# Kernel tuning notes

Hardware: AMD Instinct MI355X
Metric: run time of the kernel (lower is better)

Reference implementation:

```python
import jax, jax.numpy as jnp
from jax import lax
import numpy as np

COST_CLASS, COST_BOX, COST_GIOU = 1.0, 5.0, 2.0
B, Q, C, T = 16, 900, 92, 100
INF = jnp.float32(1e18)


def setup_inputs() -> dict:
    key = jax.random.key(0)
    k1, k2, k3, k4 = jax.random.split(key, 4)
    pred_logits = jax.random.normal(k1, (B, Q, C), jnp.float32)

    def mk_boxes(k, n):
        kc, ks = jax.random.split(k)
        cxcy = jax.random.uniform(kc, (B, n, 2), jnp.float32) * 0.8 + 0.1
        wh = jax.random.uniform(ks, (B, n, 2), jnp.float32) * 0.2 + 0.05
        return jnp.concatenate([cxcy, wh], axis=-1)  # valid cxcywh in (0,1)

    pred_boxes = mk_boxes(k2, Q)
    tgt_boxes = mk_boxes(k3, T)
    tgt_labels = jax.random.randint(k4, (B, T), 0, C)
    return {"pred_logits": pred_logits, "pred_boxes": pred_boxes,
            "tgt_labels": tgt_labels, "tgt_boxes": tgt_boxes}


def box_cxcywh_to_xyxy(b):
    cx, cy, w, h = b[..., 0], b[..., 1], b[..., 2], b[..., 3]
    return jnp.stack([cx - 0.5 * w, cy - 0.5 * h, cx + 0.5 * w, cy + 0.5 * h], axis=-1)


def generalized_box_iou(a, b):
    # a: [B,Q,4] xyxy, b: [B,T,4] xyxy -> [B,Q,T]
    area_a = (a[..., 2] - a[..., 0]) * (a[..., 3] - a[..., 1])  # [B,Q]
    area_b = (b[..., 2] - b[..., 0]) * (b[..., 3] - b[..., 1])  # [B,T]
    a_ = a[:, :, None, :]
    b_ = b[:, None, :, :]
    lt = jnp.maximum(a_[..., :2], b_[..., :2])
    rb = jnp.minimum(a_[..., 2:], b_[..., 2:])
    wh = jnp.clip(rb - lt, 0.0)
    inter = wh[..., 0] * wh[..., 1]
    union = area_a[:, :, None] + area_b[:, None, :] - inter
    iou = inter / union
    lt_c = jnp.minimum(a_[..., :2], b_[..., :2])
    rb_c = jnp.maximum(a_[..., 2:], b_[..., 2:])
    wh_c = jnp.clip(rb_c - lt_c, 0.0)
    area_c = wh_c[..., 0] * wh_c[..., 1]
    return iou - (area_c - union) / area_c


def cost_matrix(pred_logits, pred_boxes, tgt_labels, tgt_boxes):
    probs = jax.nn.softmax(pred_logits, axis=-1)                         # [B,Q,C]
    cost_class = -jnp.take_along_axis(probs, tgt_labels[:, None, :], 2)  # [B,Q,T]
    cost_box = jnp.abs(pred_boxes[:, :, None, :] - tgt_boxes[:, None, :, :]).sum(-1)
    cost_giou = -generalized_box_iou(box_cxcywh_to_xyxy(pred_boxes),
                                     box_cxcywh_to_xyxy(tgt_boxes))
    return COST_BOX * cost_box + COST_CLASS * cost_class + COST_GIOU * cost_giou


def hungarian(cost):
    # Jonker-Volgenant shortest augmenting path. cost: [n, m], n <= m, minimize.
    # Returns col_for_row [n]: column assigned to each row.
    n, m = cost.shape

    def solve_row(i, uvp):
        u, v, p = uvp  # u:[n+1] row potentials, v:[m+1] col potentials, p:[m+1] col->row (n = free)
        p = p.at[m].set(i)  # virtual start column holds current row
        minv = jnp.full((m,), INF, jnp.float32)
        way = jnp.zeros((m,), jnp.int32)
        used = jnp.zeros((m + 1,), bool)
        j0 = jnp.int32(m)

        def cond(s):
            _, _, _, _, _, j0 = s
            return p[j0] != n  # stop when a free column is reached

        def body(s):
            u, v, minv, way, used, j0 = s
            used = used.at[j0].set(True)
            i0 = p[j0]
            cur = cost[i0] - u[i0] - v[:m]           # reduced costs of row i0
            mask = (~used[:m]) & (cur < minv)
            minv = jnp.where(mask, cur, minv)
            way = jnp.where(mask, j0, way)
            mvals = jnp.where(used[:m], INF, minv)
            j1 = jnp.argmin(mvals).astype(jnp.int32)
            delta = mvals[j1]
            u = u.at[p].add(jnp.where(used, delta, 0.0))
            v = v - jnp.where(used, delta, 0.0)
            minv = jnp.where(used[:m], minv, minv - delta)
            return (u, v, minv, way, used, j1)

        u, v, minv, way, used, j0 = lax.while_loop(cond, body, (u, v, minv, way, used, j0))

        def acond(s):
            _, j0 = s
            return j0 != m

        def abody(s):
            p, j0 = s
            j1 = way[j0]
            p = p.at[j0].set(p[j1])
            return (p, j1)

        p, _ = lax.while_loop(acond, abody, (p, j0))
        return (u, v, p)

    u0 = jnp.zeros((n + 1,), jnp.float32)
    v0 = jnp.zeros((m + 1,), jnp.float32)
    p0 = jnp.full((m + 1,), n, jnp.int32)
    _, _, p = lax.fori_loop(0, n, solve_row, (u0, v0, p0))
    col_for_row = jnp.zeros((n + 1,), jnp.int32).at[p[:m]].set(
        jnp.arange(m, dtype=jnp.int32))[:n]
    return col_for_row


def reference(pred_logits, pred_boxes, tgt_labels, tgt_boxes):
    cost = cost_matrix(pred_logits, pred_boxes, tgt_labels, tgt_boxes)  # [B,Q,T]
    # assign each target (row) to a distinct query (col); vmap over batch
    q_per_t = jax.vmap(hungarian)(jnp.swapaxes(cost, 1, 2))  # [B,T]
    order = jnp.argsort(q_per_t, axis=-1)                    # sort by query idx (scipy convention)
    q_idx = jnp.take_along_axis(q_per_t, order, axis=-1)     # query indices  [B,T]
    t_idx = order.astype(jnp.int32)                          # target indices [B,T]
    return cost, q_idx, t_idx
```

## Files before the change

kernel.cpp:

```cpp
#include <hip/hip_runtime.h>

#define BB 16
#define QQ 900
#define QP 960
#define VIRT QP
#define CC 92
#define TT 100
#define INFF 1e18f
#define NK 15

#define DPP_STEP_F(x, ctrl, OP)                                             \
  do {                                                                      \
    float _o = __int_as_float(__builtin_amdgcn_update_dpp(                  \
        __float_as_int(x), __float_as_int(x), (ctrl), 0xF, 0xF, false));    \
    (x) = OP((x), _o);                                                      \
  } while (0)

#define DPP_STEP_I(x, ctrl)                                                 \
  do {                                                                      \
    int _o = __builtin_amdgcn_update_dpp((x), (x), (ctrl), 0xF, 0xF, false);\
    (x) = ((_o) < (x)) ? (_o) : (x);                                        \
  } while (0)

__device__ __forceinline__ float wave_fmin63(float x) {
  DPP_STEP_F(x, 0xB1, fminf);
  DPP_STEP_F(x, 0x4E, fminf);
  DPP_STEP_F(x, 0x141, fminf);
  DPP_STEP_F(x, 0x140, fminf);
  DPP_STEP_F(x, 0x142, fminf);
  DPP_STEP_F(x, 0x143, fminf);
  return x;
}
__device__ __forceinline__ float wave_fmax63(float x) {
  DPP_STEP_F(x, 0xB1, fmaxf);
  DPP_STEP_F(x, 0x4E, fmaxf);
  DPP_STEP_F(x, 0x141, fmaxf);
  DPP_STEP_F(x, 0x140, fmaxf);
  DPP_STEP_F(x, 0x142, fmaxf);
  DPP_STEP_F(x, 0x143, fmaxf);
  return x;
}
__device__ __forceinline__ float wave_fadd63(float x) {
#define ADDF(a, b) ((a) + (b))
  DPP_STEP_F(x, 0xB1, ADDF);
  DPP_STEP_F(x, 0x4E, ADDF);
  DPP_STEP_F(x, 0x141, ADDF);
  DPP_STEP_F(x, 0x140, ADDF);
  DPP_STEP_F(x, 0x142, ADDF);
  DPP_STEP_F(x, 0x143, ADDF);
#undef ADDF
  return x;
}
__device__ __forceinline__ int wave_imin63(int x) {
  DPP_STEP_I(x, 0xB1);
  DPP_STEP_I(x, 0x4E);
  DPP_STEP_I(x, 0x141);
  DPP_STEP_I(x, 0x140);
  DPP_STEP_I(x, 0x142);
  DPP_STEP_I(x, 0x143);
  return x;
}

__global__ __launch_bounds__(64) void cost_kernel(
    const float* __restrict__ logits,
    const float* __restrict__ pboxes,
    const int*   __restrict__ tlabels,
    const float* __restrict__ tboxes,
    float* __restrict__ cost,
    float* __restrict__ costT,
    int ctp)
{
  const int bq   = blockIdx.x;
  const int b    = bq / QQ;
  const int q    = bq - b * QQ;
  const int lane = threadIdx.x;

  __shared__ float sl[CC];

  const float a = logits[(size_t)bq * CC + lane];
  const float bb2 = (lane < CC - 64)
                        ? logits[(size_t)bq * CC + 64 + lane]
                        : -3.402823466e38f;

  float mx = fmaxf(a, bb2);
  mx = wave_fmax63(mx);
  const float m = __int_as_float(
      __builtin_amdgcn_readlane(__float_as_int(mx), 63));

  const float e0 = expf(a - m);
  const float e1 = (lane < CC - 64) ? expf(bb2 - m) : 0.0f;
  sl[lane] = e0;
  if (lane < CC - 64) sl[64 + lane] = e1;

  float sm = e0 + e1;
  sm = wave_fadd63(sm);
  const float ssum = __int_as_float(
      __builtin_amdgcn_readlane(__float_as_int(sm), 63));

  const float4 pbv = ((const float4*)pboxes)[bq];
  const float pax1 = pbv.x - 0.5f * pbv.z, pay1 = pbv.y - 0.5f * pbv.w;
  const float pax2 = pbv.x + 0.5f * pbv.z, pay2 = pbv.y + 0.5f * pbv.w;
  const float area_a = (pax2 - pax1) * (pay2 - pay1);

  for (int t = lane; t < TT; t += 64) {
    const int lab = tlabels[b * TT + t];
    const float cc = -(sl[lab] / ssum);

    const float4 tb = ((const float4*)tboxes)[b * TT + t];
    const float cbox = fabsf(pbv.x - tb.x) + fabsf(pbv.y - tb.y) +
                       fabsf(pbv.z - tb.z) + fabsf(pbv.w - tb.w);

    const float bx1 = tb.x - 0.5f * tb.z, by1 = tb.y - 0.5f * tb.w;
    const float bx2 = tb.x + 0.5f * tb.z, by2 = tb.y + 0.5f * tb.w;
    const float area_b = (bx2 - bx1) * (by2 - by1);

    const float ltx = fmaxf(pax1, bx1), lty = fmaxf(pay1, by1);
    const float rbx = fminf(pax2, bx2), rby = fminf(pay2, by2);
    const float iw = fmaxf(rbx - ltx, 0.0f), ih = fmaxf(rby - lty, 0.0f);
    const float inter = iw * ih;
    const float uni = area_a + area_b - inter;
    const float iou = inter / uni;

    const float cx1 = fminf(pax1, bx1), cy1 = fminf(pay1, by1);
    const float cx2 = fmaxf(pax2, bx2), cy2 = fmaxf(pay2, by2);
    const float cw = fmaxf(cx2 - cx1, 0.0f), ch = fmaxf(cy2 - cy1, 0.0f);
    const float ac = cw * ch;
    const float giou = iou - (ac - uni) / ac;

    const float cval = 5.0f * cbox + cc - 2.0f * giou;
    cost[(size_t)bq * TT + t] = cval;
    if (ctp) costT[((size_t)b * TT + t) * ctp + q] = cval;
  }
  if (ctp == QP && q < QP - QQ) {
    for (int t = lane; t < TT; t += 64)
      costT[((size_t)b * TT + t) * QP + QQ + q] = INFF;
  }
}

__global__ void __launch_bounds__(64, 1)
__attribute__((amdgpu_waves_per_eu(1)))
hungarianT_kernel(
    const float* __restrict__ ct,
    float* __restrict__ out_q,
    float* __restrict__ out_t)
{
  const int b    = blockIdx.x;
  const int lane = threadIdx.x;

  __shared__ int p_lds[QP + 1];
  __shared__ int way_lds[QP];
  __shared__ int qpt[TT];

  const float* __restrict__ base = ct + (size_t)b * TT * QP;

  for (int j = lane; j <= QP; j += 64) p_lds[j] = TT;

  float u0 = 0.0f, u1 = 0.0f;
  float v[NK];
#pragma unroll
  for (int k = 0; k < NK; ++k) v[k] = 0.0f;

  float c[NK];
#pragma unroll
  for (int k = 0; k < NK; ++k) c[k] = base[k * 64 + lane];

  for (int i = 0; i < TT; ++i) {
    p_lds[VIRT] = i;

    float minv[NK];
#pragma unroll
    for (int k = 0; k < NK; ++k) minv[k] = INFF;
    unsigned umask = 0;
    bool t0 = false, t1 = false;

    int i0 = i;
    int j0 = VIRT;
    int jfin;

    float us = (i0 < 64) ? u0 : u1;
    float ui0 = __int_as_float(
        __builtin_amdgcn_readlane(__float_as_int(us), i0 & 63));

    while (true) {
      t0 = t0 || (i0 == lane);
      t1 = t1 || (i0 == 64 + lane);
      if (j0 != VIRT && (j0 & 63) == lane) umask |= (1u << (j0 >> 6));

      float lmin  = INFF;
      int   kbest = 0;
#pragma unroll
      for (int k = 0; k < NK; ++k) {
        const bool  uk  = (umask >> k) & 1u;
        const float cur = c[k] - ui0 - v[k];
        const bool  imp = !uk && (cur < minv[k]);
        if (imp) { minv[k] = cur; way_lds[k * 64 + lane] = j0; }
        const float eff = uk ? INFF : minv[k];
        if (eff < lmin) { lmin = eff; kbest = k; }
      }
      const int lidx = kbest * 64 + lane;

      float red = wave_fmin63(lmin);
      const float delta = __int_as_float(
          __builtin_amdgcn_readlane(__float_as_int(red), 63));
      int cand = (lmin == delta) ? lidx : 0x7FFFFFFF;
      int redi = wave_imin63(cand);
      const int j1 = __builtin_amdgcn_readlane(redi, 63);

      int i0n = p_lds[j1];
      i0n = __builtin_amdgcn_readfirstlane(i0n);
      const bool fin = (i0n == TT);

      if (!fin) {
        const float* __restrict__ row = base + (size_t)i0n * QP;
#pragma unroll
        for (int k = 0; k < NK; ++k) c[k] = row[k * 64 + lane];
      }

      u0 += t0 ? delta : 0.0f;
      u1 += t1 ? delta : 0.0f;
#pragma unroll
      for (int k = 0; k < NK; ++k) {
        const bool uk = (umask >> k) & 1u;
        v[k]    -= uk ? delta : 0.0f;
        minv[k] -= uk ? 0.0f  : delta;
      }

      if (fin) { jfin = j1; break; }
      float us2 = (i0n < 64) ? u0 : u1;
      ui0 = __int_as_float(
          __builtin_amdgcn_readlane(__float_as_int(us2), i0n & 63));
      j0 = j1;
      i0 = i0n;
    }

    if (i + 1 < TT) {
      const float* __restrict__ row = base + (size_t)(i + 1) * QP;
#pragma unroll
      for (int k = 0; k < NK; ++k) c[k] = row[k * 64 + lane];
    }

    int j = jfin;
    while (j != VIRT) {
      const int jn = way_lds[j];
      const int pj = p_lds[jn];
      p_lds[j] = pj;
      j = jn;
    }
    asm volatile("" ::: "memory");
  }

#pragma unroll
  for (int k = 0; k < NK; ++k) {
    const int j = k * 64 + lane;
    const int r = p_lds[j];
    if (r < TT) qpt[r] = j;
  }
  __syncthreads();

  for (int t = lane; t < TT; t += 64) {
    const int myq = qpt[t];
    int rank = 0;
    for (int t2 = 0; t2 < TT; ++t2) rank += (qpt[t2] < myq) ? 1 : 0;
    out_q[b * TT + rank] = (float)myq;
    out_t[b * TT + rank] = (float)t;
  }
}

__global__ void __launch_bounds__(64)
hungarian_kernel(
    const float* __restrict__ cost,
    const float* __restrict__ costT,
    float* __restrict__ out_q,
    float* __restrict__ out_t)
{
  const int b    = blockIdx.x;
  const int lane = threadIdx.x;

  __shared__ int p_lds[QQ + 1];
  __shared__ int way_lds[QQ];
  __shared__ int qpt[TT];

  const float* base;
  size_t rs, cs;
  if (costT) { base = costT + (size_t)b * TT * QQ; rs = QQ; cs = 1; }
  else       { base = cost  + (size_t)b * QQ * TT; rs = 1;  cs = TT; }

  for (int j = lane; j <= QQ; j += 64) p_lds[j] = TT;

  float u0 = 0.0f, u1 = 0.0f;
  float v[NK];
#pragma unroll
  for (int k = 0; k < NK; ++k) v[k] = 0.0f;

  float c[NK];
#pragma unroll
  for (int k = 0; k < NK; ++k) {
    const int j = k * 64 + lane;
    c[k] = (j < QQ) ? base[(size_t)j * cs] : 0.0f;
  }

  for (int i = 0; i < TT; ++i) {
    p_lds[QQ] = i;

    float minv[NK];
#pragma unroll
    for (int k = 0; k < NK; ++k) minv[k] = INFF;
    unsigned umask = 0;
    bool t0 = false, t1 = false;

    int i0 = i;
    int j0 = QQ;
    int jfin;

    float us = (i0 < 64) ? u0 : u1;
    float ui0 = __int_as_float(
        __builtin_amdgcn_readlane(__float_as_int(us), i0 & 63));

    while (true) {
      t0 = t0 || (i0 == lane);
      t1 = t1 || (i0 == 64 + lane);
      if (j0 != QQ) {
        if ((j0 & 63) == lane) umask |= (1u << (j0 >> 6));
      }

      float lmin = INFF;
      int   lidx = QQ;
#pragma unroll
      for (int k = 0; k < NK; ++k) {
        const int j = k * 64 + lane;
        if (j < QQ && !((umask >> k) & 1u)) {
          const float cur = c[k] - ui0 - v[k];
          if (cur < minv[k]) { minv[k] = cur; way_lds[j] = j0; }
          if (minv[k] < lmin) { lmin = minv[k]; lidx = j; }
        }
      }

      float red = wave_fmin63(lmin);
      const float delta = __int_as_float(
          __builtin_amdgcn_readlane(__float_as_int(red), 63));
      int cand = (lmin == delta) ? lidx : 0x7FFFFFFF;
      int redi = wave_imin63(cand);
      const int j1 = __builtin_amdgcn_readlane(redi, 63);

      int i0n = p_lds[j1];
      i0n = __builtin_amdgcn_readfirstlane(i0n);
      const bool fin = (i0n == TT);

      u0 += t0 ? delta : 0.0f;
      u1 += t1 ? delta : 0.0f;
#pragma unroll
      for (int k = 0; k < NK; ++k) {
        const bool uk = (umask >> k) & 1u;
        v[k]    -= uk ? delta : 0.0f;
        minv[k] -= uk ? 0.0f  : delta;
      }

      if (!fin) {
        float us2 = (i0n < 64) ? u0 : u1;
        ui0 = __int_as_float(
            __builtin_amdgcn_readlane(__float_as_int(us2), i0n & 63));
#pragma unroll
        for (int k = 0; k < NK; ++k) {
          const int j = k * 64 + lane;
          if (j < QQ) c[k] = base[(size_t)i0n * rs + (size_t)j * cs];
        }
      }
      asm volatile("" ::: "memory");

      if (fin) { jfin = j1; break; }
      j0 = j1;
      i0 = i0n;
    }

    if (i + 1 < TT) {
#pragma unroll
      for (int k = 0; k < NK; ++k) {
        const int jj = k * 64 + lane;
        if (jj < QQ) c[k] = base[(size_t)(i + 1) * rs + (size_t)jj * cs];
      }
    }

    int j = jfin;
    while (j != QQ) {
      const int jn = way_lds[j];
      const int pj = p_lds[jn];
      p_lds[j] = pj;
      j = jn;
    }
    asm volatile("" ::: "memory");
  }

#pragma unroll
  for (int k = 0; k < NK; ++k) {
    const int j = k * 64 + lane;
    if (j < QQ) {
      const int r = p_lds[j];
      if (r < TT) qpt[r] = j;
    }
  }
  __syncthreads();

  for (int t = lane; t < TT; t += 64) {
    const int myq = qpt[t];
    int rank = 0;
    for (int t2 = 0; t2 < TT; ++t2) rank += (qpt[t2] < myq) ? 1 : 0;
    out_q[b * TT + rank] = (float)myq;
    out_t[b * TT + rank] = (float)t;
  }
}

extern "C" void kernel_launch(void* const* d_in, const int* in_sizes, int n_in,
                              void* d_out, int out_size, void* d_ws, size_t ws_size,
                              hipStream_t stream) {
  const float* logits  = (const float*)d_in[0];
  const float* pboxes  = (const float*)d_in[1];
  const int*   tlabels = (const int*)d_in[2];
  const float* tboxes  = (const float*)d_in[3];

  float* out  = (float*)d_out;
  float* cost = out;
  float* oq   = out + (size_t)BB * QQ * TT;
  float* ot   = oq + (size_t)BB * TT;

  const size_t padded_bytes = (size_t)BB * TT * QP * sizeof(float);
  const size_t plain_bytes  = (size_t)BB * TT * QQ * sizeof(float);

  if (ws_size >= padded_bytes) {
    float* costT = (float*)d_ws;
    hipLaunchKernelGGL(cost_kernel, dim3(BB * QQ), dim3(64), 0, stream,
                       logits, pboxes, tlabels, tboxes, cost, costT, QP);
    hipLaunchKernelGGL(hungarianT_kernel, dim3(BB), dim3(64), 0, stream,
                       costT, oq, ot);
  } else if (ws_size >= plain_bytes) {
    float* costT = (float*)d_ws;
    hipLaunchKernelGGL(cost_kernel, dim3(BB * QQ), dim3(64), 0, stream,
                       logits, pboxes, tlabels, tboxes, cost, costT, QQ);
    hipLaunchKernelGGL(hungarian_kernel, dim3(BB), dim3(64), 0, stream,
                       cost, costT, oq, ot);
  } else {
    hipLaunchKernelGGL(cost_kernel, dim3(BB * QQ), dim3(64), 0, stream,
                       logits, pboxes, tlabels, tboxes, cost, (float*)nullptr, 0);
    hipLaunchKernelGGL(hungarian_kernel, dim3(BB), dim3(64), 0, stream,
                       cost, (const float*)nullptr, oq, ot);
  }
}
```

Baseline: 190.7 us.

## Stage Hungarian cost rows into LDS asynchronously and keep assignment in packed registers

Replaces the per-step register loads of cost rows with asynchronous global-to-LDS copies into a double buffer, so the next row is fetched while the current reduction runs. The column-to-row assignment array moves from LDS into four packed byte registers per lane, read with readlane. The value min and index min reductions are merged into one 64-bit key reduction. Adds a full vmcnt wait per step, relies on byte-packed row indices below 256, and drops the single-wave occupancy hint.

```diff
diff --git a/kernel.cpp b/kernel.cpp
--- a/kernel.cpp
+++ b/kernel.cpp
@@ -16,12 +16,15 @@
     (x) = OP((x), _o);                                                      \
   } while (0)
 
-#define DPP_STEP_I(x, ctrl)                                                 \
-  do {                                                                      \
-    int _o = __builtin_amdgcn_update_dpp((x), (x), (ctrl), 0xF, 0xF, false);\
-    (x) = ((_o) < (x)) ? (_o) : (x);                                        \
-  } while (0)
-
+__device__ __forceinline__ float wave_fmax63(float x) {
+  DPP_STEP_F(x, 0xB1, fmaxf);
+  DPP_STEP_F(x, 0x4E, fmaxf);
+  DPP_STEP_F(x, 0x141, fmaxf);
+  DPP_STEP_F(x, 0x140, fmaxf);
+  DPP_STEP_F(x, 0x142, fmaxf);
+  DPP_STEP_F(x, 0x143, fmaxf);
+  return x;
+}
 __device__ __forceinline__ float wave_fmin63(float x) {
   DPP_STEP_F(x, 0xB1, fminf);
   DPP_STEP_F(x, 0x4E, fminf);
@@ -29,15 +32,6 @@
   DPP_STEP_F(x, 0x140, fminf);
   DPP_STEP_F(x, 0x142, fminf);
   DPP_STEP_F(x, 0x143, fminf);
-  return x;
-}
-__device__ __forceinline__ float wave_fmax63(float x) {
-  DPP_STEP_F(x, 0xB1, fmaxf);
-  DPP_STEP_F(x, 0x4E, fmaxf);
-  DPP_STEP_F(x, 0x141, fmaxf);
-  DPP_STEP_F(x, 0x140, fmaxf);
-  DPP_STEP_F(x, 0x142, fmaxf);
-  DPP_STEP_F(x, 0x143, fmaxf);
   return x;
 }
 __device__ __forceinline__ float wave_fadd63(float x) {
@@ -52,14 +46,63 @@
   return x;
 }
 __device__ __forceinline__ int wave_imin63(int x) {
-  DPP_STEP_I(x, 0xB1);
-  DPP_STEP_I(x, 0x4E);
-  DPP_STEP_I(x, 0x141);
-  DPP_STEP_I(x, 0x140);
-  DPP_STEP_I(x, 0x142);
-  DPP_STEP_I(x, 0x143);
+  {int _o=__builtin_amdgcn_update_dpp(x,x,0xB1,0xF,0xF,false); x=_o<x?_o:x;}
+  {int _o=__builtin_amdgcn_update_dpp(x,x,0x4E,0xF,0xF,false); x=_o<x?_o:x;}
+  {int _o=__builtin_amdgcn_update_dpp(x,x,0x141,0xF,0xF,false);x=_o<x?_o:x;}
+  {int _o=__builtin_amdgcn_update_dpp(x,x,0x140,0xF,0xF,false);x=_o<x?_o:x;}
+  {int _o=__builtin_amdgcn_update_dpp(x,x,0x142,0xF,0xF,false);x=_o<x?_o:x;}
+  {int _o=__builtin_amdgcn_update_dpp(x,x,0x143,0xF,0xF,false);x=_o<x?_o:x;}
   return x;
 }
+
+#define KEY_STEP(CTRL)                                                      \
+  do {                                                                      \
+    unsigned olo = (unsigned)__builtin_amdgcn_update_dpp(                   \
+        (int)klo, (int)klo, (CTRL), 0xF, 0xF, false);                       \
+    unsigned ohi = (unsigned)__builtin_amdgcn_update_dpp(                   \
+        (int)khi, (int)khi, (CTRL), 0xF, 0xF, false);                       \
+    const unsigned long long cur8 =                                         \
+        ((unsigned long long)khi << 32) | klo;                              \
+    const unsigned long long oth8 =                                         \
+        ((unsigned long long)ohi << 32) | olo;                              \
+    if (oth8 < cur8) { khi = ohi; klo = olo; }                              \
+  } while (0)
+
+__device__ __forceinline__ void stage_row(const float* __restrict__ row,
+                                          float* buf, int lane) {
+  typedef __attribute__((address_space(1))) const void gv_t;
+  typedef __attribute__((address_space(3))) void lv_t;
+  __builtin_amdgcn_global_load_lds((gv_t*)(row + lane * 4),       (lv_t*)(buf),       16, 0, 0);
+  __builtin_amdgcn_global_load_lds((gv_t*)(row + 256 + lane * 4), (lv_t*)(buf + 256), 16, 0, 0);
+  __builtin_amdgcn_global_load_lds((gv_t*)(row + 512 + lane * 4), (lv_t*)(buf + 512), 16, 0, 0);
+  __builtin_amdgcn_global_load_lds((gv_t*)(row + 768 + lane),     (lv_t*)(buf + 768), 4, 0, 0);
+  __builtin_amdgcn_global_load_lds((gv_t*)(row + 832 + lane),     (lv_t*)(buf + 832), 4, 0, 0);
+  __builtin_amdgcn_global_load_lds((gv_t*)(row + 896 + lane),     (lv_t*)(buf + 896), 4, 0, 0);
+}
+
+__device__ __forceinline__ int p_get(unsigned a, unsigned b, unsigned c,
+                                     unsigned d, int j) {
+  const int l = j & 63, kq = j >> 6;
+  unsigned r0 = (unsigned)__builtin_amdgcn_readlane((int)a, l);
+  unsigned r1 = (unsigned)__builtin_amdgcn_readlane((int)b, l);
+  unsigned r2 = (unsigned)__builtin_amdgcn_readlane((int)c, l);
+  unsigned r3 = (unsigned)__builtin_amdgcn_readlane((int)d, l);
+  unsigned r = (kq < 8) ? (kq < 4 ? r0 : r1) : (kq < 12 ? r2 : r3);
+  return (int)((r >> ((kq & 3) * 8)) & 0xFFu);
+}
+
+#define P_SET(jj, val)                                                      \
+  do {                                                                      \
+    const int _j = (jj); const int _kq = _j >> 6;                           \
+    const unsigned _sh = (unsigned)((_kq & 3) * 8);                         \
+    const unsigned _nm = ~(0xFFu << _sh);                                   \
+    const unsigned _in = ((unsigned)(val) & 0xFFu) << _sh;                  \
+    const bool _own = (lane == (_j & 63));                                  \
+    if (_kq < 4)       { if (_own) p4a = (p4a & _nm) | _in; }               \
+    else if (_kq < 8)  { if (_own) p4b = (p4b & _nm) | _in; }               \
+    else if (_kq < 12) { if (_own) p4c = (p4c & _nm) | _in; }               \
+    else               { if (_own) p4d = (p4d & _nm) | _in; }               \
+  } while (0)
 
 __global__ __launch_bounds__(64) void cost_kernel(
     const float* __restrict__ logits,
@@ -137,8 +180,7 @@
   }
 }
 
-__global__ void __launch_bounds__(64, 1)
-__attribute__((amdgpu_waves_per_eu(1)))
+__global__ void __launch_bounds__(64)
 hungarianT_kernel(
     const float* __restrict__ ct,
     float* __restrict__ out_q,
@@ -147,31 +189,30 @@
   const int b    = blockIdx.x;
   const int lane = threadIdx.x;
 
-  __shared__ int p_lds[QP + 1];
+  __shared__ __align__(16) float rowbuf[2][QP];
   __shared__ int way_lds[QP];
   __shared__ int qpt[TT];
 
   const float* __restrict__ base = ct + (size_t)b * TT * QP;
 
-  for (int j = lane; j <= QP; j += 64) p_lds[j] = TT;
+  unsigned p4a = 0x64646464u, p4b = 0x64646464u;
+  unsigned p4c = 0x64646464u, p4d = 0x64646464u;
 
   float u0 = 0.0f, u1 = 0.0f;
   float v[NK];
 #pragma unroll
   for (int k = 0; k < NK; ++k) v[k] = 0.0f;
 
-  float c[NK];
-#pragma unroll
-  for (int k = 0; k < NK; ++k) c[k] = base[k * 64 + lane];
+  stage_row(base, &rowbuf[0][0], lane);
 
   for (int i = 0; i < TT; ++i) {
-    p_lds[VIRT] = i;
+    float* bufc = &rowbuf[i & 1][0];
+    float* bufn = &rowbuf[(i + 1) & 1][0];
 
     float minv[NK];
 #pragma unroll
     for (int k = 0; k < NK; ++k) minv[k] = INFF;
     unsigned umask = 0;
-    bool t0 = false, t1 = false;
 
     int i0 = i;
     int j0 = VIRT;
@@ -181,48 +222,59 @@
     float ui0 = __int_as_float(
         __builtin_amdgcn_readlane(__float_as_int(us), i0 & 63));
 
-    while (true) {
-      t0 = t0 || (i0 == lane);
-      t1 = t1 || (i0 == 64 + lane);
+    for (int step = 0; step < 128; ++step) {
+      if (i0 == lane)      umask |= (1u << 30);
+      if (i0 == 64 + lane) umask |= (1u << 31);
       if (j0 != VIRT && (j0 & 63) == lane) umask |= (1u << (j0 >> 6));
+
+      asm volatile("s_waitcnt vmcnt(0)" ::: "memory");
 
       float lmin  = INFF;
       int   kbest = 0;
 #pragma unroll
       for (int k = 0; k < NK; ++k) {
+        const float ck  = bufc[k * 64 + lane];
         const bool  uk  = (umask >> k) & 1u;
-        const float cur = c[k] - ui0 - v[k];
+        const float cur = ck - ui0 - v[k];
         const bool  imp = !uk && (cur < minv[k]);
         if (imp) { minv[k] = cur; way_lds[k * 64 + lane] = j0; }
         const float eff = uk ? INFF : minv[k];
         if (eff < lmin) { lmin = eff; kbest = k; }
       }
-      const int lidx = kbest * 64 + lane;
-
-      float red = wave_fmin63(lmin);
-      const float delta = __int_as_float(
-          __builtin_amdgcn_readlane(__float_as_int(red), 63));
-      int cand = (lmin == delta) ? lidx : 0x7FFFFFFF;
-      int redi = wave_imin63(cand);
-      const int j1 = __builtin_amdgcn_readlane(redi, 63);
-
-      int i0n = p_lds[j1];
-      i0n = __builtin_amdgcn_readfirstlane(i0n);
+      const int lidx = (kbest << 6) + lane;
+
+      if (j0 == VIRT && i + 1 < TT)
+        stage_row(base + (size_t)(i + 1) * QP, bufn, lane);
+
+      unsigned fb = __float_as_uint(lmin);
+      fb = (fb & 0x80000000u) ? ~fb : (fb | 0x80000000u);
+      unsigned khi = fb, klo = (unsigned)lidx;
+      KEY_STEP(0xB1);
+      KEY_STEP(0x4E);
+      KEY_STEP(0x141);
+      KEY_STEP(0x140);
+      KEY_STEP(0x142);
+      KEY_STEP(0x143);
+      const int j1 = __builtin_amdgcn_readlane((int)klo, 63);
+      const unsigned hb =
+          (unsigned)__builtin_amdgcn_readlane((int)khi, 63);
+      const float delta =
+          __uint_as_float((hb & 0x80000000u) ? (hb ^ 0x80000000u) : ~hb);
+
+      const int  i0n = p_get(p4a, p4b, p4c, p4d, j1);
       const bool fin = (i0n == TT);
 
+      if (!fin) stage_row(base + (size_t)i0n * QP, bufc, lane);
+
+      u0 += ((umask >> 30) & 1u) ? delta : 0.0f;
+      u1 += (umask >> 31)        ? delta : 0.0f;
+#pragma unroll
+      for (int k = 0; k < NK; ++k)
+        v[k] -= ((umask >> k) & 1u) ? delta : 0.0f;
       if (!fin) {
-        const float* __restrict__ row = base + (size_t)i0n * QP;
-#pragma unroll
-        for (int k = 0; k < NK; ++k) c[k] = row[k * 64 + lane];
-      }
-
-      u0 += t0 ? delta : 0.0f;
-      u1 += t1 ? delta : 0.0f;
-#pragma unroll
-      for (int k = 0; k < NK; ++k) {
-        const bool uk = (umask >> k) & 1u;
-        v[k]    -= uk ? delta : 0.0f;
-        minv[k] -= uk ? 0.0f  : delta;
+#pragma unroll
+        for (int k = 0; k < NK; ++k)
+          minv[k] -= ((umask >> k) & 1u) ? 0.0f : delta;
       }
 
       if (fin) { jfin = j1; break; }
@@ -233,26 +285,25 @@
       i0 = i0n;
     }
 
-    if (i + 1 < TT) {
-      const float* __restrict__ row = base + (size_t)(i + 1) * QP;
-#pragma unroll
-      for (int k = 0; k < NK; ++k) c[k] = row[k * 64 + lane];
-    }
-
-    int j = jfin;
-    while (j != VIRT) {
-      const int jn = way_lds[j];
-      const int pj = p_lds[jn];
-      p_lds[j] = pj;
-      j = jn;
-    }
-    asm volatile("" ::: "memory");
+    if (j0 == VIRT) {
+      P_SET(jfin, i);
+    } else {
+      int j = jfin;
+      for (int hop = 0; hop < 128 && j != VIRT; ++hop) {
+        int jn = way_lds[j];
+        jn = __builtin_amdgcn_readfirstlane(jn);
+        const int pj = (jn == VIRT) ? i : p_get(p4a, p4b, p4c, p4d, jn);
+        P_SET(j, pj);
+        j = jn;
+      }
+    }
   }
 
 #pragma unroll
   for (int k = 0; k < NK; ++k) {
+    const unsigned reg = (k < 4) ? p4a : (k < 8) ? p4b : (k < 12) ? p4c : p4d;
+    const int r = (int)((reg >> ((k & 3) * 8)) & 0xFFu);
     const int j = k * 64 + lane;
-    const int r = p_lds[j];
     if (r < TT) qpt[r] = j;
   }
   __syncthreads();
```

After: 219.3 us. +15.0%, slower.
